# Kernel optimization log

Measured on AMD Instinct MI355X. Metric: run time of the kernel, lower is better.

## Reference

```python
import jax, jax.numpy as jnp
import numpy as np

INPUT_DIM = 512
HIDDEN_DIM = 512


def _linear_params(key, in_dim, out_dim):
    kw, kb = jax.random.split(key)
    bound = 1.0 / np.sqrt(in_dim)
    W = jax.random.uniform(kw, (out_dim, in_dim), minval=-bound, maxval=bound, dtype=jnp.float32)
    b = jax.random.uniform(kb, (out_dim,), minval=-bound, maxval=bound, dtype=jnp.float32)
    return W, b


def setup_inputs() -> dict:
    key = jax.random.key(0)
    keys = jax.random.split(key, 11)
    B = 8192
    inp = {
        "x_t": jax.random.normal(keys[0], (B, INPUT_DIM), dtype=jnp.float32),
        "h_tm1": jax.random.normal(keys[1], (B, HIDDEN_DIM), dtype=jnp.float32),
        "c_tm1": jax.random.normal(keys[2], (B, HIDDEN_DIM), dtype=jnp.float32),
    }
    names = ["f_x", "f_h", "i_x", "i_h", "g_x", "g_h", "o_x", "o_h"]
    for n, k in zip(names, keys[3:]):
        in_dim = INPUT_DIM if n.endswith("_x") else HIDDEN_DIM
        W, b = _linear_params(k, in_dim, HIDDEN_DIM)
        inp[f"W_{n}"] = W
        inp[f"b_{n}"] = b
    return inp


def reference(x_t, h_tm1, c_tm1,
              W_f_x, b_f_x, W_f_h, b_f_h,
              W_i_x, b_i_x, W_i_h, b_i_h,
              W_g_x, b_g_x, W_g_h, b_g_h,
              W_o_x, b_o_x, W_o_h, b_o_h):
    # Stacked weights: [4, H, D] -> einsum over D gives [B, 4, H].
    Wx = jnp.stack([W_f_x, W_g_x, W_i_x, W_o_x])  # [4, H, Din]
    bx = jnp.stack([b_f_x, b_g_x, b_i_x, b_o_x])  # [4, H]
    Wh = jnp.stack([W_f_h, W_g_h, W_i_h, W_o_h])
    bh = jnp.stack([b_f_h, b_g_h, b_i_h, b_o_h])
    pre = (jnp.einsum('bd,ghd->bgh', x_t, Wx) + bx
           + jnp.einsum('bd,ghd->bgh', h_tm1, Wh) + bh)  # [B, 4, H]
    f_t = jax.nn.sigmoid(pre[:, 0])
    g_t = jnp.tanh(pre[:, 1])
    i_t = jax.nn.sigmoid(pre[:, 2])
    o_t = jax.nn.sigmoid(pre[:, 3])
    c_t = f_t * c_tm1 + i_t * g_t
    h_t = o_t * jnp.tanh(c_t)
    return (h_t, c_t)
```

## Files before the change

### kernel.cpp

```cpp
#include <hip/hip_runtime.h>
#include <cstdint>
#include <cstddef>


typedef __attribute__((ext_vector_type(8))) short short8;
typedef __attribute__((ext_vector_type(4))) float floatx4;

#define AS1(p) ((const __attribute__((address_space(1))) void*)(p))
#define AS3(p) ((__attribute__((address_space(3))) void*)(p))

__device__ __forceinline__ unsigned short f2bf(float f) {
  union { float f; unsigned u; } v; v.f = f;
  unsigned u = v.u;
  return (unsigned short)((u + 0x7fffu + ((u >> 16) & 1u)) >> 16);
}

struct PackArgs {
  const float* x; const float* h;
  const float* wx[4]; const float* wh[4];
  const float* bx[4]; const float* bh[4];
  unsigned short* A; unsigned short* B; float* bias;
};

__global__ __launch_bounds__(256) void pack_all_kernel(PackArgs P) {
  const int bid = blockIdx.x;
  if (bid < 8192) {
    int e = (bid * 256 + threadIdx.x) * 4;
    int b = e >> 10, k = e & 1023;
    const float* src = (k < 512) ? (P.x + b * 512 + k)
                                 : (P.h + b * 512 + (k - 512));
    float4 v = *(const float4*)src;
    ushort4 o;
    o.x = f2bf(v.x); o.y = f2bf(v.y); o.z = f2bf(v.z); o.w = f2bf(v.w);
    *(ushort4*)(P.A + e) = o;
  } else {
    int e = ((bid - 8192) * 256 + threadIdx.x) * 4;
    int n = e >> 10, k = e & 1023;
    int g = n & 3, hh = n >> 2;
    const float* src = (k < 512) ? (P.wx[g] + hh * 512 + k)
                                 : (P.wh[g] + hh * 512 + (k - 512));
    float4 v = *(const float4*)src;
    ushort4 o;
    o.x = f2bf(v.x); o.y = f2bf(v.y); o.z = f2bf(v.z); o.w = f2bf(v.w);
    *(ushort4*)(P.B + e) = o;
    if (k == 0) P.bias[n] = P.bx[g][hh] + P.bh[g][hh];
  }
}

__global__ __launch_bounds__(512, 4)
void lstm_gemm_kernel(const unsigned short* __restrict__ A,
                      const unsigned short* __restrict__ B,
                      const float* __restrict__ bias,
                      const float* __restrict__ c_prev,
                      float* __restrict__ h_out,
                      float* __restrict__ c_out) {
  __shared__ __align__(16) char smem[49152];
  __shared__ __align__(16) float biasS[128];

  const int tid  = threadIdx.x;
  const int lane = tid & 63;
  const int w    = tid >> 6;
  const int quad = lane >> 4;
  const int colA = lane & 15;
  const int m0   = blockIdx.x * 256;
  const int n0   = blockIdx.y * 128;
  const int h0   = blockIdx.y * 32;

  if (tid < 128) biasS[tid] = bias[n0 + tid];

  const int srow = tid >> 3;
  const int cl   = tid & 7;
  const int cg   = cl ^ (srow & 7);

  floatx4 acc[4][4];
#pragma unroll
  for (int i = 0; i < 4; ++i)
#pragma unroll
    for (int j = 0; j < 4; ++j) acc[i][j] = (floatx4){0.f, 0.f, 0.f, 0.f};

  const int wm = (w >> 1) * 64;
  const int wn = (w & 1) * 64;

  const char* Ag = (const char*)A;
  const char* Bg = (const char*)B;

  for (int kt = 0; kt < 16; ++kt) {
    __syncthreads();
    const int kb = kt * 128;
#pragma unroll
    for (int j = 0; j < 4; ++j) {
      int r = j * 64 + srow;
      __builtin_amdgcn_global_load_lds(
          AS1(Ag + (size_t)(m0 + r) * 2048 + kb + cg * 16),
          AS3(smem + r * 128 + cl * 16), 16, 0, 0);
    }
#pragma unroll
    for (int j = 0; j < 2; ++j) {
      int r = j * 64 + srow;
      __builtin_amdgcn_global_load_lds(
          AS1(Bg + (size_t)(n0 + r) * 2048 + kb + cg * 16),
          AS3(smem + 32768 + r * 128 + cl * 16), 16, 0, 0);
    }
    __syncthreads();

#pragma unroll
    for (int kk = 0; kk < 2; ++kk) {
      const int off = ((kk * 4 + quad) ^ (colA & 7)) * 16;
      short8 af[4], bfr[4];
#pragma unroll
      for (int mi = 0; mi < 4; ++mi)
        af[mi] = *(const short8*)(smem + (wm + mi * 16 + colA) * 128 + off);
#pragma unroll
      for (int ni = 0; ni < 4; ++ni)
        bfr[ni] = *(const short8*)(smem + 32768 + (wn + ni * 16 + colA) * 128 + off);
#pragma unroll
      for (int mi = 0; mi < 4; ++mi)
#pragma unroll
        for (int ni = 0; ni < 4; ++ni)
          acc[mi][ni] = __builtin_amdgcn_mfma_f32_16x16x32_bf16(
              af[mi], bfr[ni], acc[mi][ni], 0, 0, 0);
    }
  }

  __syncthreads();
  float* ep = (float*)smem;
#pragma unroll
  for (int rd = 0; rd < 4; ++rd) {
    float cp[4];
#pragma unroll
    for (int j = 0; j < 4; ++j) {
      int idx  = j * 512 + tid;
      int mloc = idx >> 5;
      int hh   = idx & 31;
      cp[j] = c_prev[(m0 + rd * 64 + mloc) * 512 + h0 + hh];
    }
    if ((w >> 1) == rd) {
#pragma unroll
      for (int mi = 0; mi < 4; ++mi)
#pragma unroll
        for (int ni = 0; ni < 4; ++ni) {
          int rr0 = mi * 16 + quad * 4;
          int cc  = wn + ni * 16 + colA;
#pragma unroll
          for (int rr = 0; rr < 4; ++rr)
            ep[(rr0 + rr) * 132 + cc] = acc[mi][ni][rr];
        }
    }
    __syncthreads();
#pragma unroll
    for (int j = 0; j < 4; ++j) {
      int idx  = j * 512 + tid;
      int mloc = idx >> 5;
      int hh   = idx & 31;
      float4 pre = *(const float4*)(ep + mloc * 132 + hh * 4);
      float4 bb  = *(const float4*)(biasS + hh * 4);
      float pf = pre.x + bb.x;
      float pi = pre.y + bb.y;
      float pg = pre.z + bb.z;
      float po = pre.w + bb.w;
      float fg = 1.f / (1.f + __expf(-pf));
      float ig = 1.f / (1.f + __expf(-pi));
      float gg = 1.f - 2.f / (1.f + __expf(2.f * pg));
      float og = 1.f / (1.f + __expf(-po));
      float cv = fg * cp[j] + ig * gg;
      float th = 1.f - 2.f / (1.f + __expf(2.f * cv));
      int m  = m0 + rd * 64 + mloc;
      int hg = h0 + hh;
      h_out[m * 512 + hg] = og * th;
      c_out[m * 512 + hg] = cv;
    }
    __syncthreads();
  }
}

extern "C" void kernel_launch(void* const* d_in, const int* in_sizes, int n_in,
                              void* d_out, int out_size, void* d_ws, size_t ws_size,
                              hipStream_t stream) {
  char* ws = (char*)d_ws;
  unsigned short* Abf = (unsigned short*)ws;
  unsigned short* Bbf = (unsigned short*)(ws + (size_t)16777216);
  float* bias = (float*)(ws + (size_t)16777216 + 4194304);

  float* hout = (float*)d_out;
  float* cout = hout + (size_t)8192 * 512;

  PackArgs P;
  P.x = (const float*)d_in[0];
  P.h = (const float*)d_in[1];
  P.wx[0] = (const float*)d_in[3];  P.bx[0] = (const float*)d_in[4];
  P.wh[0] = (const float*)d_in[5];  P.bh[0] = (const float*)d_in[6];
  P.wx[1] = (const float*)d_in[7];  P.bx[1] = (const float*)d_in[8];
  P.wh[1] = (const float*)d_in[9];  P.bh[1] = (const float*)d_in[10];
  P.wx[2] = (const float*)d_in[11]; P.bx[2] = (const float*)d_in[12];
  P.wh[2] = (const float*)d_in[13]; P.bh[2] = (const float*)d_in[14];
  P.wx[3] = (const float*)d_in[15]; P.bx[3] = (const float*)d_in[16];
  P.wh[3] = (const float*)d_in[17]; P.bh[3] = (const float*)d_in[18];
  P.A = Abf; P.B = Bbf; P.bias = bias;

  pack_all_kernel<<<10240, 256, 0, stream>>>(P);

  const float* c = (const float*)d_in[2];
  dim3 grid(32, 16);
  lstm_gemm_kernel<<<grid, 512, 0, stream>>>(Abf, Bbf, bias, c, hout, cout);
}
```

Baseline: 167.2 us.

## Double-buffer LDS tiles with K=64 stages to overlap loads with MFMA

Replaces the single-buffered K=128 tile loop (two barriers per step) with a double-buffered K=64 pipeline. The next stage's global-to-LDS loads are issued before the current stage's MFMAs, and there is one barrier per iteration. A new XOR swizzle is used for the 64-byte rows. The aim is to hide global load latency behind compute. In exchange the loop runs twice as many iterations with less MFMA work per barrier.

```diff
diff --git a/kernel.cpp b/kernel.cpp
--- a/kernel.cpp
+++ b/kernel.cpp
@@ -68,61 +68,58 @@
 
   if (tid < 128) biasS[tid] = bias[n0 + tid];
 
-  const int srow = tid >> 3;
-  const int cl   = tid & 7;
-  const int cg   = cl ^ (srow & 7);
-
-  floatx4 acc[4][4];
-#pragma unroll
-  for (int i = 0; i < 4; ++i)
-#pragma unroll
-    for (int j = 0; j < 4; ++j) acc[i][j] = (floatx4){0.f, 0.f, 0.f, 0.f};
-
   const int wm = (w >> 1) * 64;
   const int wn = (w & 1) * 64;
 
+  const int sR   = tid >> 2;
+  const int cs16 = ((tid & 3) ^ ((tid >> 3) & 3)) * 16;
+  const int swzF = (quad ^ ((colA >> 1) & 3)) * 16;
+
   const char* Ag = (const char*)A;
   const char* Bg = (const char*)B;
 
-  for (int kt = 0; kt < 16; ++kt) {
+  floatx4 acc[4][4];
+#pragma unroll
+  for (int i = 0; i < 4; ++i)
+#pragma unroll
+    for (int j = 0; j < 4; ++j) acc[i][j] = (floatx4){0.f, 0.f, 0.f, 0.f};
+
+  auto stage = [&](int ktt, int bb) {
+    const int kb   = ktt * 64;
+    const int base = bb * 24576;
+#pragma unroll
+    for (int j = 0; j < 2; ++j)
+      __builtin_amdgcn_global_load_lds(
+          AS1(Ag + (size_t)(m0 + j * 128 + sR) * 2048 + kb + cs16),
+          AS3(smem + base + j * 8192 + tid * 16), 16, 0, 0);
+    __builtin_amdgcn_global_load_lds(
+        AS1(Bg + (size_t)(n0 + sR) * 2048 + kb + cs16),
+        AS3(smem + base + 16384 + tid * 16), 16, 0, 0);
+  };
+
+  stage(0, 0);
+  __syncthreads();
+
+  for (int kt = 0; kt < 32; ++kt) {
+    const int bb   = kt & 1;
+    const int base = bb * 24576;
+    if (kt < 31) stage(kt + 1, bb ^ 1);
+    short8 af[4], bfr[4];
+#pragma unroll
+    for (int mi = 0; mi < 4; ++mi)
+      af[mi] = *(const short8*)(smem + base + (wm + mi * 16 + colA) * 64 + swzF);
+#pragma unroll
+    for (int ni = 0; ni < 4; ++ni)
+      bfr[ni] = *(const short8*)(smem + base + 16384 + (wn + ni * 16 + colA) * 64 + swzF);
+#pragma unroll
+    for (int mi = 0; mi < 4; ++mi)
+#pragma unroll
+      for (int ni = 0; ni < 4; ++ni)
+        acc[mi][ni] = __builtin_amdgcn_mfma_f32_16x16x32_bf16(
+            af[mi], bfr[ni], acc[mi][ni], 0, 0, 0);
     __syncthreads();
-    const int kb = kt * 128;
-#pragma unroll
-    for (int j = 0; j < 4; ++j) {
-      int r = j * 64 + srow;
-      __builtin_amdgcn_global_load_lds(
-          AS1(Ag + (size_t)(m0 + r) * 2048 + kb + cg * 16),
-          AS3(smem + r * 128 + cl * 16), 16, 0, 0);
-    }
-#pragma unroll
-    for (int j = 0; j < 2; ++j) {
-      int r = j * 64 + srow;
-      __builtin_amdgcn_global_load_lds(
-          AS1(Bg + (size_t)(n0 + r) * 2048 + kb + cg * 16),
-          AS3(smem + 32768 + r * 128 + cl * 16), 16, 0, 0);
-    }
-    __syncthreads();
-
-#pragma unroll
-    for (int kk = 0; kk < 2; ++kk) {
-      const int off = ((kk * 4 + quad) ^ (colA & 7)) * 16;
-      short8 af[4], bfr[4];
-#pragma unroll
-      for (int mi = 0; mi < 4; ++mi)
-        af[mi] = *(const short8*)(smem + (wm + mi * 16 + colA) * 128 + off);
-#pragma unroll
-      for (int ni = 0; ni < 4; ++ni)
-        bfr[ni] = *(const short8*)(smem + 32768 + (wn + ni * 16 + colA) * 128 + off);
-#pragma unroll
-      for (int mi = 0; mi < 4; ++mi)
-#pragma unroll
-        for (int ni = 0; ni < 4; ++ni)
-          acc[mi][ni] = __builtin_amdgcn_mfma_f32_16x16x32_bf16(
-              af[mi], bfr[ni], acc[mi][ni], 0, 0, 0);
-    }
   }
 
-  __syncthreads();
   float* ep = (float*)smem;
 #pragma unroll
   for (int rd = 0; rd < 4; ++rd) {
```

Result: slower. 170.7 us (+2.1%).
